# Optimization experiments

Measured on AMD Instinct MI355X. Metric: run time of the kernel, lower is better.

Reference implementation:

```python
import jax, jax.numpy as jnp
import numpy as np
import math

B, T, NC = 16, 256, 2
_NS = (9, 9, 11, 11, 9, 20)  # legacy6 region node counts
_OUT, _RF, _FD, _NH, _FF = 32, 64, 128, 4, 2048


def _region_adj(n):
    # chain + second-order edges (legacy6), plus self-loops; GCN sym-normalized
    A = np.zeros((n, n), np.float32)
    for i in range(n - 1):
        A[i, i + 1] = A[i + 1, i] = 1.0
    for i in range(n - 2):
        A[i, i + 2] = A[i + 2, i] = 1.0
    A = A + np.eye(n, dtype=np.float32)
    d = A.sum(1) ** -0.5
    return jnp.asarray(d[:, None] * A * d[None, :])

_ADJS = [_region_adj(n) for n in _NS]


def _pe_table(t, d):
    pos = np.arange(t, dtype=np.float32)[:, None]
    div = np.exp(np.arange(0, d, 2, dtype=np.float32) * (-math.log(10000.0) / d))
    pe = np.zeros((t, d), np.float32)
    pe[:, 0::2] = np.sin(pos * div)
    pe[:, 1::2] = np.cos(pos * div)
    return jnp.asarray(pe)

_PE = _pe_table(T, _FD)


def _ln(x, g, b, eps=1e-5):
    m = jnp.mean(x, -1, keepdims=True)
    v = jnp.mean((x - m) ** 2, -1, keepdims=True)
    return (x - m) / jnp.sqrt(v + eps) * g + b


def _mha(q, kv, qkv_w, qkv_b, ow, ob, nh):
    d = q.shape[-1]
    hd = d // nh
    wq, wk, wv = jnp.split(qkv_w, 3, axis=1)
    bq, bk, bv = jnp.split(qkv_b, 3)
    def sp(x):
        return x.reshape(x.shape[0], x.shape[1], nh, hd).transpose(0, 2, 1, 3)
    Q, K, V = sp(q @ wq + bq), sp(kv @ wk + bk), sp(kv @ wv + bv)
    att = jax.nn.softmax(jnp.einsum('bhqd,bhkd->bhqk', Q, K) / jnp.sqrt(jnp.float32(hd)), axis=-1)
    o = jnp.einsum('bhqk,bhkd->bhqd', att, V).transpose(0, 2, 1, 3).reshape(q.shape[0], q.shape[1], d)
    return o @ ow + ob


def _tel(x, qkv_w, qkv_b, ow, ob, l1g, l1b, f1w, f1b, f2w, f2b, l2g, l2b, nh):
    # torch post-norm TransformerEncoderLayer (relu FFN, eval mode: no dropout)
    x = _ln(x + _mha(x, x, qkv_w, qkv_b, ow, ob, nh), l1g, l1b)
    ff = jax.nn.relu(x @ f1w + f1b) @ f2w + f2b
    return _ln(x + ff, l2g, l2b)


def setup_inputs() -> dict:
    key = jax.random.key(0)
    ks = iter(jax.random.split(key, 80))
    def nrm(shape, s=0.05):
        return jax.random.normal(next(ks), shape, jnp.float32) * s
    inp = {}
    for name, n in zip(('x_ljaw', 'x_rjaw', 'x_leye', 'x_reye', 'x_nose', 'x_mouth'), _NS):
        inp[name] = jax.random.normal(next(ks), (B, T, n, 11), jnp.float32)
    inp['global_feats'] = jax.random.normal(next(ks), (B, T, 4), jnp.float32)
    inp['global_alpha'] = jnp.float32(0.2)
    inp['gcn1_w'] = nrm((6, 11, _OUT)); inp['gcn1_b'] = jnp.zeros((6, _OUT))
    inp['gcn2_w'] = nrm((6, _OUT, _OUT)); inp['gcn2_b'] = jnp.zeros((6, _OUT))
    inp['rln_g'] = jnp.ones((6, _RF)); inp['rln_b'] = jnp.zeros((6, _RF))
    inp['sp_qkv_w'] = nrm((_RF, 3 * _RF)); inp['sp_qkv_b'] = jnp.zeros((3 * _RF,))
    inp['sp_out_w'] = nrm((_RF, _RF)); inp['sp_out_b'] = jnp.zeros((_RF,))
    inp['sp_ln1_g'] = jnp.ones((_RF,)); inp['sp_ln1_b'] = jnp.zeros((_RF,))
    inp['sp_ff1_w'] = nrm((_RF, _FF)); inp['sp_ff1_b'] = jnp.zeros((_FF,))
    inp['sp_ff2_w'] = nrm((_FF, _RF)); inp['sp_ff2_b'] = jnp.zeros((_RF,))
    inp['sp_ln2_g'] = jnp.ones((_RF,)); inp['sp_ln2_b'] = jnp.zeros((_RF,))
    priors = np.array([0.3, 0.3, 0.8, 0.8, 0.4, 1.0], np.float32)
    inp['region_logits'] = jnp.asarray(np.log(np.expm1(priors)).reshape(1, 6, 1))
    inp['gate1_w'] = nrm((_RF, 32)); inp['gate1_b'] = jnp.zeros((32,))
    inp['gate2_w'] = nrm((32, 1)); inp['gate2_b'] = jnp.zeros((1,))
    inp['ca_qkv_w'] = nrm((_RF, 3 * _RF)); inp['ca_qkv_b'] = jnp.zeros((3 * _RF,))
    inp['ca_out_w'] = nrm((_RF, _RF)); inp['ca_out_b'] = jnp.zeros((_RF,))
    inp['ca_ln_g'] = jnp.ones((_RF,)); inp['ca_ln_b'] = jnp.zeros((_RF,))
    inp['glob_w'] = nrm((4, _RF)); inp['glob_b'] = jnp.zeros((_RF,))
    inp['glob_ln_g'] = jnp.ones((_RF,)); inp['glob_ln_b'] = jnp.zeros((_RF,))
    inp['fused_ln_g'] = jnp.ones((_FD,)); inp['fused_ln_b'] = jnp.zeros((_FD,))
    inp['tp_qkv_w'] = nrm((_FD, 3 * _FD)); inp['tp_qkv_b'] = jnp.zeros((3 * _FD,))
    inp['tp_out_w'] = nrm((_FD, _FD)); inp['tp_out_b'] = jnp.zeros((_FD,))
    inp['tp_ln1_g'] = jnp.ones((_FD,)); inp['tp_ln1_b'] = jnp.zeros((_FD,))
    inp['tp_ff1_w'] = nrm((_FD, _FF)); inp['tp_ff1_b'] = jnp.zeros((_FF,))
    inp['tp_ff2_w'] = nrm((_FF, _FD)); inp['tp_ff2_b'] = jnp.zeros((_FD,))
    inp['tp_ln2_g'] = jnp.ones((_FD,)); inp['tp_ln2_b'] = jnp.zeros((_FD,))
    inp['attnproj_w'] = nrm((_FD, 1)); inp['attnproj_b'] = jnp.zeros((1,))
    inp['cls1_w'] = nrm((_FD, _OUT)); inp['cls1_b'] = jnp.zeros((_OUT,))
    inp['cls_ln_g'] = jnp.ones((_OUT,)); inp['cls_ln_b'] = jnp.zeros((_OUT,))
    inp['cls2_w'] = nrm((_OUT, NC)); inp['cls2_b'] = jnp.zeros((NC,))
    return inp


def reference(x_ljaw, x_rjaw, x_leye, x_reye, x_nose, x_mouth, global_feats, global_alpha, gcn1_w, gcn1_b, gcn2_w, gcn2_b, rln_g, rln_b, sp_qkv_w, sp_qkv_b, sp_out_w, sp_out_b, sp_ln1_g, sp_ln1_b, sp_ff1_w, sp_ff1_b, sp_ff2_w, sp_ff2_b, sp_ln2_g, sp_ln2_b, region_logits, gate1_w, gate1_b, gate2_w, gate2_b, ca_qkv_w, ca_qkv_b, ca_out_w, ca_out_b, ca_ln_g, ca_ln_b, glob_w, glob_b, glob_ln_g, glob_ln_b, fused_ln_g, fused_ln_b, tp_qkv_w, tp_qkv_b, tp_out_w, tp_out_b, tp_ln1_g, tp_ln1_b, tp_ff1_w, tp_ff1_b, tp_ff2_w, tp_ff2_b, tp_ln2_g, tp_ln2_b, attnproj_w, attnproj_b, cls1_w, cls1_b, cls_ln_g, cls_ln_b, cls2_w, cls2_b):
    xs = (x_ljaw, x_rjaw, x_leye, x_reye, x_nose, x_mouth)
    Bc, Tc = x_ljaw.shape[0], x_ljaw.shape[1]
    # per-region 2-layer GCN + concat(mean,max) node pooling -> (B,T,64) tokens
    toks = []
    for i in range(6):
        A = _ADJS[i]
        h = jax.nn.relu(jnp.einsum('nm,btmf->btnf', A, xs[i] @ gcn1_w[i]) + gcn1_b[i])
        h = jax.nn.relu(jnp.einsum('nm,btmf->btnf', A, h @ gcn2_w[i]) + gcn2_b[i])
        feat = jnp.concatenate([h.mean(2), h.max(2)], -1)
        toks.append(_ln(feat, rln_g[i], rln_b[i]))
    tok = jnp.stack(toks, 2).reshape(Bc * Tc, 6, _RF)
    # spatial transformer over the 6 region tokens per frame
    tok = _tel(tok, sp_qkv_w, sp_qkv_b, sp_out_w, sp_out_b, sp_ln1_g, sp_ln1_b, sp_ff1_w, sp_ff1_b, sp_ff2_w, sp_ff2_b, sp_ln2_g, sp_ln2_b, _NH)
    # learned region priors (softplus) * per-sample sigmoid gates
    rw = jax.nn.softplus(region_logits)
    gate = jax.nn.sigmoid(jax.nn.relu(tok @ gate1_w + gate1_b) @ gate2_w + gate2_b)
    tok = tok * rw * gate
    # cross-attn fusion: mean-region query attends over region tokens
    q = jnp.mean(tok, 1, keepdims=True)
    attn = _mha(q, tok, ca_qkv_w, ca_qkv_b, ca_out_w, ca_out_b, _NH)
    fused_r = _ln(q[:, 0] + attn[:, 0], ca_ln_g, ca_ln_b)
    # gated global branch (4 -> 64), concat to fused_dim=128
    g = jax.nn.relu(_ln(global_feats.reshape(Bc * Tc, 4) @ glob_w + glob_b, glob_ln_g, glob_ln_b))
    g = jnp.tanh(global_alpha) * g
    fused = _ln(jnp.concatenate([fused_r, g], -1), fused_ln_g, fused_ln_b).reshape(Bc, Tc, _FD)
    # temporal transformer + attention pooling over time
    fused = fused + _PE[None, :Tc]
    h = _tel(fused, tp_qkv_w, tp_qkv_b, tp_out_w, tp_out_b, tp_ln1_g, tp_ln1_b, tp_ff1_w, tp_ff1_b, tp_ff2_w, tp_ff2_b, tp_ln2_g, tp_ln2_b, _NH)
    wt = jax.nn.softmax(h @ attnproj_w + attnproj_b, axis=1)
    pooled = jnp.sum(wt * h, 1)
    z = jax.nn.relu(_ln(pooled @ cls1_w + cls1_b, cls_ln_g, cls_ln_b))
    return z @ cls2_w + cls2_b
```

## Files before the change

### kernel.cpp

```cpp
#include <hip/hip_runtime.h>
#include <math.h>
#include <stddef.h>

#define NFRM 4096
#define NBATCH 16

typedef __attribute__((ext_vector_type(8))) short short8v;
typedef __attribute__((ext_vector_type(4))) float f32x4;
#define MFMA_BF16(a,b,c) __builtin_amdgcn_mfma_f32_16x16x32_bf16(a,b,c,0,0,0)

__device__ inline float wsum64(float v){
  #pragma unroll
  for(int m=32;m>=1;m>>=1) v += __shfl_xor(v, m, 64);
  return v;
}

__device__ inline float pe_val(int t,int d){
  int k = d >> 1;
  float div = expf(-(float)(2*k) * (9.210340371976184f/128.f));
  float ang = (float)t * div;
  return (d & 1) ? cosf(ang) : sinf(ang);
}

__device__ inline void bf16split(float x, unsigned short &h, unsigned short &l){
// ... 30 lines not shown
    const float* __restrict__ b1,
    const unsigned short* __restrict__ w2h, const unsigned short* __restrict__ w2l)
{
  constexpr int TM=32, JC=128;
  constexpr int KS1 = D/32;
  constexpr int NT2W = (D/16)/4;
  constexpr int HS = 2048/NS;
  constexpr int NCH = HS/JC;
  constexpr int HP = JC + 8;
  __shared__ unsigned short Hh[TM][HP];
  __shared__ unsigned short Hl[TM][HP];
  int tid = threadIdx.x;
  int lane = tid & 63, w = tid >> 6;
  int ar = lane & 15, ak = lane >> 4;
  size_t Ntok = (size_t)gridDim.x*TM;
  const float* Xb = X + (size_t)blockIdx.x*TM*D;

  short8v xah[2][KS1], xal[2][KS1];
  #pragma unroll
  for(int mt=0;mt<2;mt++){
    #pragma unroll
    for(int s=0;s<KS1;s++){
      const float* xp = Xb + (size_t)(mt*16+ar)*D + s*32 + ak*8;
      #pragma unroll
      for(int e=0;e<8;e++){
        unsigned short h,l;
        bf16split(xp[e],h,l);
        xah[mt][s][e]=(short)h; xal[mt][s][e]=(short)l;
      }
    }
  }

  f32x4 acc2[2][NT2W];
  #pragma unroll
  for(int mt=0;mt<2;mt++)
    #pragma unroll
    for(int nt=0;nt<NT2W;nt++)
      acc2[mt][nt] = (f32x4){0.f,0.f,0.f,0.f};

  for(int ch=0; ch<NCH; ch++){
    int jc = blockIdx.y*HS + ch*JC;
    f32x4 a1[2][2];
    #pragma unroll
    for(int mt=0;mt<2;mt++){ a1[mt][0]=(f32x4){0,0,0,0}; a1[mt][1]=(f32x4){0,0,0,0}; }
    #pragma unroll
    for(int s=0;s<KS1;s++){
      #pragma unroll
      for(int nt=0;nt<2;nt++){
        int ntile1 = (jc + w*32 + nt*16) >> 4;
        size_t off = (((size_t)ntile1*KS1 + s)*64 + lane)*8;
        short8v bh = *(const short8v*)(w1h + off);
        short8v bl = *(const short8v*)(w1l + off);
        #pragma unroll
        for(int mt=0;mt<2;mt++){
          a1[mt][nt] = MFMA_BF16(xah[mt][s], bh, a1[mt][nt]);
          a1[mt][nt] = MFMA_BF16(xah[mt][s], bl, a1[mt][nt]);
          a1[mt][nt] = MFMA_BF16(xal[mt][s], bh, a1[mt][nt]);
        }
      }
    }
    __syncthreads();
    #pragma unroll
    for(int nt=0;nt<2;nt++){
      int colBase = w*32 + nt*16 + ar;
      float bval = b1[jc + colBase];
      #pragma unroll
      for(int mt=0;mt<2;mt++){
        #pragma unroll
        for(int r=0;r<4;r++){
          float hv = a1[mt][nt][r] + bval;
          hv = fmaxf(hv, 0.f);
          unsigned short h,l;
          bf16split(hv,h,l);
          int row = mt*16 + ak*4 + r;
          Hh[row][colBase]=h; Hl[row][colBase]=l;
        }
      }
    }
    __syncthreads();
    #pragma unroll
    for(int s2=0;s2<4;s2++){
      short8v ah[2], al[2];
      #pragma unroll
      for(int mt=0;mt<2;mt++){
        ah[mt] = *(const short8v*)&Hh[mt*16+ar][s2*32 + ak*8];
        al[mt] = *(const short8v*)&Hl[mt*16+ar][s2*32 + ak*8];
      }
      #pragma unroll
      for(int nt=0;nt<NT2W;nt++){
        int ntile2 = w*NT2W + nt;
        int kstep2 = (jc >> 5) + s2;
        size_t off = (((size_t)ntile2*64 + kstep2)*64 + lane)*8;
        short8v bh = *(const short8v*)(w2h + off);
        short8v bl = *(const short8v*)(w2l + off);
        #pragma unroll
        for(int mt=0;mt<2;mt++){
          acc2[mt][nt] = MFMA_BF16(ah[mt], bh, acc2[mt][nt]);
          acc2[mt][nt] = MFMA_BF16(ah[mt], bl, acc2[mt][nt]);
          acc2[mt][nt] = MFMA_BF16(al[mt], bh, acc2[mt][nt]);
        }
      }
    }
  }
  float* Pb = P + (size_t)blockIdx.y*Ntok*D + (size_t)blockIdx.x*TM*D;
  #pragma unroll
  for(int mt=0;mt<2;mt++){
    #pragma unroll
    for(int nt=0;nt<NT2W;nt++){
      int col = (w*NT2W + nt)*16 + ar;
      #pragma unroll
      for(int r=0;r<4;r++){
        int row = mt*16 + ak*4 + r;
        Pb[(size_t)row*D + col] = acc2[mt][nt][r];
      }
    }
  }
}

template<int D, int NS>
__global__ __launch_bounds__(256) void ffn_combine_kernel(
    const float* __restrict__ X, const float* __restrict__ P,
    float* __restrict__ Y,
    const float* __restrict__ b2,
    const float* __restrict__ lg, const float* __restrict__ lb)
{
  constexpr int EPL = D/64;
  int tid=threadIdx.x;
  int lane = tid & 63;
  size_t Ntok = (size_t)gridDim.x*4;
  size_t row = (size_t)blockIdx.x*4 + (tid>>6);
  size_t base = row*D;
  float e[EPL];
  float s=0.f;
  #pragma unroll
  for(int i=0;i<EPL;i++){
    int c = i*64+lane;
    float v = X[base+c] + b2[c];
    #pragma unroll
    for(int sp=0;sp<NS;sp++) v += P[(size_t)sp*Ntok*D + base + c];
    e[i]=v; s+=v;
  }
  float mm = wsum64(s)*(1.f/D);
  float s2=0.f;
  #pragma unroll
  for(int i=0;i<EPL;i++){ float d=e[i]-mm; s2+=d*d; }
  float rs = rsqrtf(wsum64(s2)*(1.f/D)+1e-5f);
  #pragma unroll
  for(int i=0;i<EPL;i++){
    int c=i*64+lane;
    Y[base+c] = (e[i]-mm)*rs*lg[c]+lb[c];
  }
}

__global__ __launch_bounds__(64) void gcn_kernel(
    const float* __restrict__ x0,const float* __restrict__ x1,
    const float* __restrict__ x2,const float* __restrict__ x3,
    const float* __restrict__ x4,const float* __restrict__ x5,
    const float* __restrict__ g1w,const float* __restrict__ g1b,
    const float* __restrict__ g2w,const float* __restrict__ g2b,
    const float* __restrict__ rg,const float* __restrict__ rb,
    float* __restrict__ tok)
{
  int f = blockIdx.x;
  int r = blockIdx.y;
  int tid = threadIdx.x;
  int n = (r==5) ? 20 : ((r==2 || r==3) ? 11 : 9);
  const float* xr = (r==0)?x0:(r==1)?x1:(r==2)?x2:(r==3)?x3:(r==4)?x4:x5;
  const float* W1 = g1w + r*11*32;
  const float* b1 = g1b + r*32;
  const float* W2 = g2w + r*32*32;
  const float* b2 = g2b + r*32;

  __shared__ float xs[20*11];
  __shared__ float t0[20*32];
  __shared__ float t1[20*32];

  for(int i=tid;i<n*11;i+=64) xs[i] = xr[(size_t)f*n*11 + i];
  __syncthreads();
  for(int i=tid;i<n*32;i+=64){
    int node=i>>5, c=i&31;
    float s=0.f;
    #pragma unroll
    for(int k=0;k<11;k++) s += xs[node*11+k]*W1[k*32+c];
    t0[i]=s;
  }
  __syncthreads();
  for(int i=tid;i<n*32;i+=64){
    int node=i>>5, c=i&31;
    int di = 1 + min(node,2) + min(n-1-node,2);
    float s=b1[c];
    int lo = max(node-2,0), hi = min(node+2,n-1);
    for(int m=lo;m<=hi;m++){
      int dm = 1 + min(m,2) + min(n-1-m,2);
      s += rsqrtf((float)(di*dm)) * t0[m*32+c];
    }
    t1[i]=fmaxf(s,0.f);
  }
  __syncthreads();
  for(int i=tid;i<n*32;i+=64){
    int node=i>>5, c=i&31;
    float s=0.f;
    #pragma unroll
    for(int k=0;k<32;k++) s += t1[node*32+k]*W2[k*32+c];
    t0[i]=s;
  }
  __syncthreads();
  for(int i=tid;i<n*32;i+=64){
    int node=i>>5, c=i&31;
    int di = 1 + min(node,2) + min(n-1-node,2);
    float s=b2[c];
    int lo = max(node-2,0), hi = min(node+2,n-1);
    for(int m=lo;m<=hi;m++){
      int dm = 1 + min(m,2) + min(n-1-m,2);
      s += rsqrtf((float)(di*dm)) * t0[m*32+c];
    }
    t1[i]=fmaxf(s,0.f);
  }
  __syncthreads();
  float v;
  if(tid<32){
    float s=0.f;
    for(int m=0;m<n;m++) s += t1[m*32+tid];
    v = s/(float)n;
  } else {
    int c=tid-32;
    float mx=-1e30f;
    for(int m=0;m<n;m++) mx = fmaxf(mx, t1[m*32+c]);
    v = mx;
  }
  float m1 = wsum64(v)*(1.f/64.f);
  float d1 = v - m1;
  float var = wsum64(d1*d1)*(1.f/64.f);
  float y = d1*rsqrtf(var+1e-5f)*rg[r*64+tid] + rb[r*64+tid];
  tok[((size_t)f*6+r)*64+tid] = y;
}

__global__ __launch_bounds__(64) void sp_attn_kernel(
    float* __restrict__ tok,
    const float* __restrict__ qkvw,const float* __restrict__ qkvb,
    const float* __restrict__ ow,const float* __restrict__ ob,
    const float* __restrict__ l1g,const float* __restrict__ l1b)
{
  int f=blockIdx.x, tid=threadIdx.x;
  __shared__ float Xv[384];
  __shared__ float QKV[1152];
  __shared__ float SC[144];
  __shared__ float AO[384];
  __shared__ float Yv[384];
  float* trow = tok + (size_t)f*384;
  for(int i=tid;i<384;i+=64) Xv[i]=trow[i];
  __syncthreads();
  for(int i=tid;i<1152;i+=64){
    int tk=i/192, c=i%192;
    float s=qkvb[c];
    #pragma unroll
    for(int k=0;k<64;k++) s += Xv[tk*64+k]*qkvw[k*192+c];
    QKV[i]=s;
  }
  __syncthreads();
  for(int i=tid;i<144;i+=64){
    int h=i/36, qi=(i%36)/6, ki=i%6;
    float s=0.f;
    #pragma unroll
    for(int d=0;d<16;d++) s += QKV[qi*192+h*16+d]*QKV[ki*192+64+h*16+d];
    SC[i]=s*0.25f;
  }
  __syncthreads();
  if(tid<24){
    int base=(tid/6)*36+(tid%6)*6;
    float mx=-1e30f;
    for(int k=0;k<6;k++) mx=fmaxf(mx,SC[base+k]);
    float sm=0.f;
    for(int k=0;k<6;k++){ float e=expf(SC[base+k]-mx); SC[base+k]=e; sm+=e; }
    float rr=1.f/sm;
    for(int k=0;k<6;k++) SC[base+k]*=rr;
  }
  __syncthreads();
  for(int i=tid;i<384;i+=64){
    int tk=i/64, c=i%64, h=c/16;
    float s=0.f;
    #pragma unroll
    for(int k=0;k<6;k++) s += SC[h*36+tk*6+k]*QKV[k*192+128+c];
    AO[i]=s;
  }
  __syncthreads();
  for(int i=tid;i<384;i+=64){
    int tk=i/64, c=i%64;
    float s=ob[c];
    #pragma unroll
    for(int k=0;k<64;k++) s += AO[tk*64+k]*ow[k*64+c];
    Yv[i]=Xv[i]+s;
  }
  __syncthreads();
  #pragma unroll
  for(int row=0;row<6;row++){
    float v=Yv[row*64+tid];
    float mm=wsum64(v)*(1.f/64.f);
    float d=v-mm;
    float var=wsum64(d*d)*(1.f/64.f);
    trow[row*64+tid]=d*rsqrtf(var+1e-5f)*l1g[tid]+l1b[tid];
  }
}

template<int D, int TM>
__global__ __launch_bounds__(256) void ffn_ln_kernel(
    const float* __restrict__ X, float* __restrict__ Yout,
    const float* __restrict__ w1,const float* __restrict__ b1,
    const float* __restrict__ w2,const float* __restrict__ b2,
    const float* __restrict__ lg,const float* __restrict__ lb)
{
  constexpr int JC = 128;
  constexpr int JS = JC + 4;
  constexpr int M1 = TM/8;
  constexpr int CG = D/4;
  constexpr int MG2 = 256/CG;
  constexpr int M2 = TM/MG2;
  __shared__ float Xs[TM*D];
  __shared__ float Hs[TM*JS];
  int tid=threadIdx.x;
  const float* Xb = X + (size_t)blockIdx.x*TM*D;
  for(int i=tid;i<TM*D;i+=256) Xs[i]=Xb[i];

  int jg = tid & 31, j0 = jg*4;
  int mg1 = tid >> 5;
  int m10 = mg1*M1;
  int cg = tid % CG, c0 = cg*4;
  int mg2 = tid / CG;
  int m20 = mg2*M2;

  float acc[M2][4];
  #pragma unroll
  for(int m=0;m<M2;m++){ acc[m][0]=0.f;acc[m][1]=0.f;acc[m][2]=0.f;acc[m][3]=0.f; }

  __syncthreads();
  for(int jc=0;jc<2048;jc+=JC){
    float a1[M1][4];
    float4 bv = *(const float4*)&b1[jc+j0];
    #pragma unroll
    for(int m=0;m<M1;m++){ a1[m][0]=bv.x;a1[m][1]=bv.y;a1[m][2]=bv.z;a1[m][3]=bv.w; }
    for(int k0=0;k0<D;k0+=4){
      float4 wr0 = *(const float4*)&w1[(size_t)(k0+0)*2048 + jc + j0];
      float4 wr1 = *(const float4*)&w1[(size_t)(k0+1)*2048 + jc + j0];
      float4 wr2 = *(const float4*)&w1[(size_t)(k0+2)*2048 + jc + j0];
      float4 wr3 = *(const float4*)&w1[(size_t)(k0+3)*2048 + jc + j0];
      #pragma unroll
      for(int m=0;m<M1;m++){
        float4 xv = *(const float4*)&Xs[(m10+m)*D + k0];
        a1[m][0] += xv.x*wr0.x + xv.y*wr1.x + xv.z*wr2.x + xv.w*wr3.x;
        a1[m][1] += xv.x*wr0.y + xv.y*wr1.y + xv.z*wr2.y + xv.w*wr3.y;
        a1[m][2] += xv.x*wr0.z + xv.y*wr1.z + xv.z*wr2.z + xv.w*wr3.z;
        a1[m][3] += xv.x*wr0.w + xv.y*wr1.w + xv.z*wr2.w + xv.w*wr3.w;
      }
    }
    #pragma unroll
    for(int m=0;m<M1;m++){
      float4 hv;
      hv.x=fmaxf(a1[m][0],0.f); hv.y=fmaxf(a1[m][1],0.f);
      hv.z=fmaxf(a1[m][2],0.f); hv.w=fmaxf(a1[m][3],0.f);
      *(float4*)&Hs[(m10+m)*JS + j0] = hv;
    }
    __syncthreads();
    for(int jj0=0;jj0<JC;jj0+=4){
      float4 w20 = *(const float4*)&w2[(size_t)(jc+jj0+0)*D + c0];
      float4 w21 = *(const float4*)&w2[(size_t)(jc+jj0+1)*D + c0];
      float4 w22 = *(const float4*)&w2[(size_t)(jc+jj0+2)*D + c0];
      float4 w23 = *(const float4*)&w2[(size_t)(jc+jj0+3)*D + c0];
      #pragma unroll
      for(int m=0;m<M2;m++){
        float4 hv = *(const float4*)&Hs[(m20+m)*JS + jj0];
        acc[m][0] += hv.x*w20.x + hv.y*w21.x + hv.z*w22.x + hv.w*w23.x;
        acc[m][1] += hv.x*w20.y + hv.y*w21.y + hv.z*w22.y + hv.w*w23.y;
        acc[m][2] += hv.x*w20.z + hv.y*w21.z + hv.z*w22.z + hv.w*w23.z;
        acc[m][3] += hv.x*w20.w + hv.y*w21.w + hv.z*w22.w + hv.w*w23.w;
      }
    }
    __syncthreads();
  }
  {
    float4 b2v = *(const float4*)&b2[c0];
    #pragma unroll
    for(int m=0;m<M2;m++){
      int row = m20+m;
      float4 xv = *(const float4*)&Xs[row*D + c0];
      float4 yv;
      yv.x = xv.x + acc[m][0] + b2v.x;
      yv.y = xv.y + acc[m][1] + b2v.y;
      yv.z = xv.z + acc[m][2] + b2v.z;
      yv.w = xv.w + acc[m][3] + b2v.w;
      *(float4*)&Hs[row*D + c0] = yv;
    }
  }
  __syncthreads();
  constexpr int EPL = D/64;
  int lane = tid & 63, wv = tid >> 6;
  float* Yb = Yout + (size_t)blockIdx.x*TM*D;
  for(int row=wv; row<TM; row+=4){
    float e[EPL];
    float s=0.f;
    #pragma unroll
    for(int i=0;i<EPL;i++){ e[i]=Hs[row*D + i*64 + lane]; s+=e[i]; }
    float mm = wsum64(s)*(1.f/D);
    float s2=0.f;
    #pragma unroll
    for(int i=0;i<EPL;i++){ float d=e[i]-mm; s2+=d*d; }
    float rs = rsqrtf(wsum64(s2)*(1.f/D)+1e-5f);
    #pragma unroll
    for(int i=0;i<EPL;i++)
      Yb[row*D + i*64 + lane] = (e[i]-mm)*rs*lg[i*64+lane]+lb[i*64+lane];
  }
}

__global__ __launch_bounds__(64) void fuse_kernel(
    const float* __restrict__ tok, const float* __restrict__ gfeat,
    const float* __restrict__ alpha_p, const float* __restrict__ rlogit,
    const float* __restrict__ g1w,const float* __restrict__ g1b,
    const float* __restrict__ g2w,const float* __restrict__ g2b,
    const float* __restrict__ caqw,const float* __restrict__ caqb,
    const float* __restrict__ caow,const float* __restrict__ caob,
    const float* __restrict__ calng,const float* __restrict__ calnb,
    const float* __restrict__ gw,const float* __restrict__ gb,
    const float* __restrict__ glng,const float* __restrict__ glnb,
    const float* __restrict__ flng,const float* __restrict__ flnb,
    float* __restrict__ fused)
{
  int f=blockIdx.x, tid=threadIdx.x;
  __shared__ float X[384];
  __shared__ float G1[192];
  __shared__ float gt[6];
  __shared__ float qv[64];
  __shared__ float Qs[64];
  __shared__ float KK[384], VV[384];
  __shared__ float sc[24];
  __shared__ float AOs[64];

  const float* trow = tok + (size_t)f*384;
  for(int i=tid;i<384;i+=64) X[i]=trow[i];
  __syncthreads();
  for(int i=tid;i<192;i+=64){
    int rr=i/32, j=i%32;
    float s=g1b[j];
    #pragma unroll
    for(int k=0;k<64;k++) s += X[rr*64+k]*g1w[k*32+j];
    G1[i]=fmaxf(s,0.f);
  }
  __syncthreads();
  if(tid<6){
    float s=g2b[0];
    #pragma unroll
    for(int k=0;k<32;k++) s += G1[tid*32+k]*g2w[k];
    float gate = 1.f/(1.f+expf(-s));
    float rw = log1pf(expf(rlogit[tid]));
    gt[tid]=gate*rw;
  }
  __syncthreads();
  for(int i=tid;i<384;i+=64) X[i]*=gt[i/64];
  __syncthreads();
  {
    float s=0.f;
    #pragma unroll
    for(int rr=0;rr<6;rr++) s+=X[rr*64+tid];
    qv[tid]=s*(1.f/6.f);
  }
  __syncthreads();
  {
    float s=caqb[tid];
    #pragma unroll
    for(int k=0;k<64;k++) s += qv[k]*caqw[k*192+tid];
    Qs[tid]=s;
  }
  for(int i=tid;i<384;i+=64){
    int rr=i/64, c=i%64;
    float sk=caqb[64+c], sv=caqb[128+c];
    #pragma unroll
    for(int k=0;k<64;k++){
      float xv=X[rr*64+k];
      sk += xv*caqw[k*192+64+c];
      sv += xv*caqw[k*192+128+c];
    }
    KK[i]=sk; VV[i]=sv;
  }
  __syncthreads();
  if(tid<24){
    int h=tid/6, ki=tid%6;
    float s=0.f;
    #pragma unroll
    for(int d=0;d<16;d++) s += Qs[h*16+d]*KK[ki*64+h*16+d];
    sc[tid]=s*0.25f;
  }
  __syncthreads();
  if(tid<4){
    float mx=-1e30f;
    for(int k=0;k<6;k++) mx=fmaxf(mx,sc[tid*6+k]);
    float sm=0.f;
    for(int k=0;k<6;k++){ float e=expf(sc[tid*6+k]-mx); sc[tid*6+k]=e; sm+=e; }
    float rr=1.f/sm;
    for(int k=0;k<6;k++) sc[tid*6+k]*=rr;
  }
  __syncthreads();
  {
    int h=tid/16;
    float s=0.f;
    #pragma unroll
    for(int k=0;k<6;k++) s += sc[h*6+k]*VV[k*64+tid];
    AOs[tid]=s;
  }
  __syncthreads();
  float pr;
  {
    float s=caob[tid];
    #pragma unroll
    for(int k=0;k<64;k++) s += AOs[k]*caow[k*64+tid];
    pr = qv[tid] + s;
  }
  float m1=wsum64(pr)*(1.f/64.f);
  float d1=pr-m1;
  float v1=wsum64(d1*d1)*(1.f/64.f);
  float fr = d1*rsqrtf(v1+1e-5f)*calng[tid]+calnb[tid];
  float gvv;
  {
    float s=gb[tid];
    #pragma unroll
    for(int k=0;k<4;k++) s += gfeat[(size_t)f*4+k]*gw[k*64+tid];
    gvv=s;
  }
  float m2=wsum64(gvv)*(1.f/64.f);
  float d2=gvv-m2;
  float v2=wsum64(d2*d2)*(1.f/64.f);
  float gg = fmaxf(d2*rsqrtf(v2+1e-5f)*glng[tid]+glnb[tid],0.f)*tanhf(alpha_p[0]);
  float sm_ = wsum64(fr+gg)*(1.f/128.f);
  float da=fr-sm_, db=gg-sm_;
  float vv = wsum64(da*da+db*db)*(1.f/128.f);
  float rs = rsqrtf(vv+1e-5f);
  int t = f & 255;
  fused[(size_t)f*128+tid]     = da*rs*flng[tid]+flnb[tid]         + pe_val(t,tid);
  fused[(size_t)f*128+64+tid]  = db*rs*flng[64+tid]+flnb[64+tid]   + pe_val(t,64+tid);
}

__global__ __launch_bounds__(256) void tqkv_gemm_kernel(
    const float* __restrict__ X, float* __restrict__ Y,
    const float* __restrict__ w, const float* __restrict__ b)
{
  __shared__ float Xs[32*128];
  int tid=threadIdx.x;
  const float* Xb = X + (size_t)blockIdx.x*32*128;
  for(int i=tid;i<4096;i+=256) Xs[i]=Xb[i];
  __syncthreads();
  int cg = tid & 31, c0 = cg*4;
  int mg = tid >> 5, m0 = mg*4;
  float* Yb = Y + (size_t)blockIdx.x*32*384;
  int oc = blockIdx.y*128;
  float acc[4][4];
  float4 bv = *(const float4*)&b[oc+c0];
  #pragma unroll
  for(int m=0;m<4;m++){ acc[m][0]=bv.x;acc[m][1]=bv.y;acc[m][2]=bv.z;acc[m][3]=bv.w; }
  for(int k0=0;k0<128;k0+=4){
    float4 w0 = *(const float4*)&w[(k0+0)*384 + oc + c0];
    float4 w1 = *(const float4*)&w[(k0+1)*384 + oc + c0];
    float4 w2 = *(const float4*)&w[(k0+2)*384 + oc + c0];
    float4 w3 = *(const float4*)&w[(k0+3)*384 + oc + c0];
    #pragma unroll
    for(int m=0;m<4;m++){
      float4 xv = *(const float4*)&Xs[(m0+m)*128 + k0];
      acc[m][0] += xv.x*w0.x + xv.y*w1.x + xv.z*w2.x + xv.w*w3.x;
      acc[m][1] += xv.x*w0.y + xv.y*w1.y + xv.z*w2.y + xv.w*w3.y;
      acc[m][2] += xv.x*w0.z + xv.y*w1.z + xv.z*w2.z + xv.w*w3.z;
      acc[m][3] += xv.x*w0.w + xv.y*w1.w + xv.z*w2.w + xv.w*w3.w;
    }
  }
  #pragma unroll
  for(int m=0;m<4;m++){
    float4 yv; yv.x=acc[m][0];yv.y=acc[m][1];yv.z=acc[m][2];yv.w=acc[m][3];
    *(float4*)&Yb[(m0+m)*384 + oc + c0] = yv;
  }
}

__global__ __launch_bounds__(256) void tattn_split_kernel(
    const float* __restrict__ qkv, float* __restrict__ PO,
    float* __restrict__ PM, float* __restrict__ PL)
{
  int b=blockIdx.x, h=blockIdx.y, s=blockIdx.z, tid=threadIdx.x;
  __shared__ float Ksh[32*32];
  __shared__ float Vsh[32*32];
  const float* base = qkv + (size_t)b*256*384;
  int k0 = s*32;
  for(int i=tid;i<1024;i+=256){
    int t=i>>5, d=i&31;
    Ksh[i]=base[(size_t)(k0+t)*384+128+h*32+d];
    Vsh[i]=base[(size_t)(k0+t)*384+256+h*32+d];
  }
  float q[32];
  #pragma unroll
  for(int d=0;d<32;d++) q[d]=base[(size_t)tid*384+h*32+d];
  __syncthreads();
  const float scale=0.17677669529663687f;
  float sc[32];
  float mx=-1e30f;
  #pragma unroll
  for(int k=0;k<32;k++){
    float sv=0.f;
    #pragma unroll
    for(int d=0;d<32;d++) sv += q[d]*Ksh[k*32+d];
    sc[k]=sv*scale;
    mx=fmaxf(mx,sc[k]);
  }
  float l=0.f, o[32];
  #pragma unroll
  for(int d=0;d<32;d++) o[d]=0.f;
  #pragma unroll
  for(int k=0;k<32;k++){
    float p=expf(sc[k]-mx);
    l+=p;
    #pragma unroll
    for(int d=0;d<32;d++) o[d]+=p*Vsh[k*32+d];
  }
  int bh = b*4+h;
  size_t idx = ((size_t)s*64 + bh)*256 + tid;
  PM[idx]=mx; PL[idx]=l;
  float* po = PO + idx*32;
  #pragma unroll
  for(int d=0;d<32;d++) po[d]=o[d];
}

__global__ __launch_bounds__(256) void attn_combine_kernel(
    const float* __restrict__ PO, const float* __restrict__ PM,
    const float* __restrict__ PL, float* __restrict__ obuf)
{
  int tid=threadIdx.x;
  int ql = tid>>5, d = tid&31;
  int bh = blockIdx.x >> 5;
  int qc = blockIdx.x & 31;
  int q = qc*8 + ql;
  float ms[8], ls[8];
  float M=-1e30f;
  #pragma unroll
  for(int s=0;s<8;s++){
    size_t idx = ((size_t)s*64 + bh)*256 + q;
    ms[s]=PM[idx]; ls[s]=PL[idx];
    M=fmaxf(M,ms[s]);
  }
  float L=0.f, ov=0.f;
  #pragma unroll
  for(int s=0;s<8;s++){
    float w = expf(ms[s]-M);
    L += ls[s]*w;
    size_t idx = ((size_t)s*64 + bh)*256 + q;
    ov += w * PO[idx*32 + d];
  }
  int b = bh>>2, h = bh&3;
  obuf[(size_t)(b*256+q)*128 + h*32 + d] = ov / L;
}

__global__ __launch_bounds__(256) void tattn_kernel(
    const float* __restrict__ qkv, float* __restrict__ obuf)
{
  int b=blockIdx.x, h=blockIdx.y, tid=threadIdx.x;
  __shared__ float Ksh[256*32];
  __shared__ float Vsh[64*32];
  const float* base = qkv + (size_t)b*256*384;
  for(int i=tid;i<8192;i+=256){
    int t=i>>5, d=i&31;
    Ksh[i]=base[t*384+128+h*32+d];
  }
  float q[32];
  #pragma unroll
  for(int d=0;d<32;d++) q[d]=base[(size_t)tid*384+h*32+d];
  __syncthreads();
  const float scale=0.17677669529663687f;
  float mx=-1e30f;
  for(int k=0;k<256;k++){
    float s=0.f;
    #pragma unroll
    for(int d=0;d<32;d++) s += q[d]*Ksh[k*32+d];
    mx=fmaxf(mx,s*scale);
  }
  float l=0.f, o[32];
  #pragma unroll
  for(int d=0;d<32;d++) o[d]=0.f;
  for(int kc=0;kc<256;kc+=64){
    __syncthreads();
    for(int i=tid;i<2048;i+=256){
      int t=i>>5, d=i&31;
      Vsh[i]=base[(size_t)(kc+t)*384+256+h*32+d];
    }
    __syncthreads();
    for(int k2=0;k2<64;k2++){
      float s=0.f;
      #pragma unroll
      for(int d=0;d<32;d++) s += q[d]*Ksh[(kc+k2)*32+d];
// ... 75 lines not shown
  __shared__ float invs[1];
  __shared__ float pooled[128];
  __shared__ float z[32];
  const float* H = h2 + (size_t)b*256*128;
  {
    float s=apb[0];
    #pragma unroll
    for(int k=0;k<128;k++) s += H[(size_t)tid*128+k]*apw[k];
    lg[tid]=s;
  }
  __syncthreads();
  if(tid==0){
    float mx=-1e30f;
    for(int i=0;i<256;i++) mx=fmaxf(mx,lg[i]);
    float sm=0.f;
    for(int i=0;i<256;i++){ float e=expf(lg[i]-mx); wt[i]=e; sm+=e; }
    invs[0]=1.f/sm;
  }
  __syncthreads();
  float inv=invs[0];
  if(tid<128){
    float s=0.f;
    for(int t=0;t<256;t++) s += wt[t]*inv*H[(size_t)t*128+tid];
    pooled[tid]=s;
  }
  __syncthreads();
  if(tid<32){
    float s=c1b[tid];
    #pragma unroll
    for(int k=0;k<128;k++) s += pooled[k]*c1w[k*32+tid];
    z[tid]=s;
  }
  __syncthreads();
  if(tid==0){
    float m=0.f;
    for(int i=0;i<32;i++) m+=z[i];
    m *= (1.f/32.f);
    float v=0.f;
    for(int i=0;i<32;i++){ float d=z[i]-m; v+=d*d; }
    v *= (1.f/32.f);
    float rs=rsqrtf(v+1e-5f);
    for(int i=0;i<32;i++) z[i]=fmaxf((z[i]-m)*rs*clng[i]+clnb[i],0.f);
  }
  __syncthreads();
  if(tid<2){
    float s=c2b[tid];
    #pragma unroll
    for(int k=0;k<32;k++) s += z[k]*c2w[k*2+tid];
    out[b*2+tid]=s;
  }
}

extern "C" void kernel_launch(void* const* d_in, const int* in_sizes, int n_in,
                              void* d_out, int out_size, void* d_ws, size_t ws_size,
                              hipStream_t stream) {
  const float* x0 = (const float*)d_in[0];
  const float* x1 = (const float*)d_in[1];
  const float* x2 = (const float*)d_in[2];
  const float* x3 = (const float*)d_in[3];
  const float* x4 = (const float*)d_in[4];
  const float* x5 = (const float*)d_in[5];
  const float* gfeat   = (const float*)d_in[6];
  const float* alpha_p = (const float*)d_in[7];
  const float* g1w = (const float*)d_in[8];
  const float* g1b = (const float*)d_in[9];
  const float* g2w = (const float*)d_in[10];
  const float* g2b = (const float*)d_in[11];
  const float* rlg = (const float*)d_in[12];
  const float* rlb = (const float*)d_in[13];
  const float* spqkvw = (const float*)d_in[14];
  const float* spqkvb = (const float*)d_in[15];
  const float* spow = (const float*)d_in[16];
  const float* spob = (const float*)d_in[17];
  const float* spl1g = (const float*)d_in[18];
  const float* spl1b = (const float*)d_in[19];
  const float* spf1w = (const float*)d_in[20];
  const float* spf1b = (const float*)d_in[21];
  const float* spf2w = (const float*)d_in[22];
  const float* spf2b = (const float*)d_in[23];
  const float* spl2g = (const float*)d_in[24];
  const float* spl2b = (const float*)d_in[25];
  const float* rlogit = (const float*)d_in[26];
  const float* gate1w = (const float*)d_in[27];
  const float* gate1b = (const float*)d_in[28];
  const float* gate2w = (const float*)d_in[29];
  const float* gate2b = (const float*)d_in[30];
  const float* caqkvw = (const float*)d_in[31];
  const float* caqkvb = (const float*)d_in[32];
  const float* caow = (const float*)d_in[33];
  const float* caob = (const float*)d_in[34];
  const float* calng = (const float*)d_in[35];
  const float* calnb = (const float*)d_in[36];
  const float* globw = (const float*)d_in[37];
  const float* globb = (const float*)d_in[38];
  const float* glng = (const float*)d_in[39];
  const float* glnb = (const float*)d_in[40];
  const float* flng = (const float*)d_in[41];
  const float* flnb = (const float*)d_in[42];
  const float* tpqkvw = (const float*)d_in[43];
  const float* tpqkvb = (const float*)d_in[44];
  const float* tpow = (const float*)d_in[45];
  const float* tpob = (const float*)d_in[46];
  const float* tpl1g = (const float*)d_in[47];
  const float* tpl1b = (const float*)d_in[48];
  const float* tpf1w = (const float*)d_in[49];
  const float* tpf1b = (const float*)d_in[50];
  const float* tpf2w = (const float*)d_in[51];
  const float* tpf2b = (const float*)d_in[52];
  const float* tpl2g = (const float*)d_in[53];
  const float* tpl2b = (const float*)d_in[54];
  const float* apw = (const float*)d_in[55];
  const float* apb = (const float*)d_in[56];
  const float* c1w = (const float*)d_in[57];
  const float* c1b = (const float*)d_in[58];
  const float* clng = (const float*)d_in[59];
  const float* clnb = (const float*)d_in[60];
  const float* c2w = (const float*)d_in[61];
  const float* c2b = (const float*)d_in[62];

  float* ws = (float*)d_ws;
  float* tok   = ws;
  float* fused = tok   + (size_t)NFRM*384;
  float* qkv   = fused + (size_t)NFRM*128;
  float* obuf  = qkv   + (size_t)NFRM*384;
  float* part  = obuf  + (size_t)NFRM*128;
  size_t part_elems = (size_t)2*24576*64;
  unsigned short* pk = (unsigned short*)(part + part_elems);
  unsigned short* sp1h = pk;
  unsigned short* sp1l = sp1h + 131072;
  unsigned short* sp2h = sp1l + 131072;
  unsigned short* sp2l = sp2h + 131072;
  unsigned short* tp1h = sp2l + 131072;
  unsigned short* tp1l = tp1h + 262144;
  unsigned short* tp2h = tp1l + 262144;
  unsigned short* tp2l = tp2h + 262144;
  size_t pack_ushorts = 4*131072 + 4*262144;
  size_t need = ((size_t)NFRM*384 + NFRM*128 + NFRM*384 + NFRM*128 + part_elems)*4
              + pack_ushorts*2;
  bool mfma_ok = (ws_size >= need);

  float* attnPO = (float*)(pk + pack_ushorts);
  float* attnPM = attnPO + (size_t)8*64*256*32;
  float* attnPL = attnPM + (size_t)8*64*256;
  size_t need2 = need + ((size_t)8*64*256*32 + 2*(size_t)8*64*256)*4;
  bool attn_ok = (ws_size >= need2);

  if(mfma_ok){
    pack_w_kernel<<<dim3(128,2),64,0,stream>>>(spf1w, sp1h, sp1l, 64, 2048);
    pack_w_kernel<<<dim3(4,64),64,0,stream>>>(spf2w, sp2h, sp2l, 2048, 64);
    pack_w_kernel<<<dim3(128,4),64,0,stream>>>(tpf1w, tp1h, tp1l, 128, 2048);
    pack_w_kernel<<<dim3(8,64),64,0,stream>>>(tpf2w, tp2h, tp2l, 2048, 128);
  }

  gcn_kernel<<<dim3(NFRM,6),64,0,stream>>>(x0,x1,x2,x3,x4,x5,g1w,g1b,g2w,g2b,rlg,rlb,tok);
  sp_attn_kernel<<<NFRM,64,0,stream>>>(tok,spqkvw,spqkvb,spow,spob,spl1g,spl1b);
  if(mfma_ok){
    ffn_mfma_partial<64,2><<<dim3(768,2),256,0,stream>>>(tok,part,sp1h,sp1l,spf1b,sp2h,sp2l);
    ffn_combine_kernel<64,2><<<24576/4,256,0,stream>>>(tok,part,tok,spf2b,spl2g,spl2b);
  } else {
    ffn_ln_kernel<64,32><<<768,256,0,stream>>>(tok,tok,spf1w,spf1b,spf2w,spf2b,spl2g,spl2b);
  }
  fuse_kernel<<<NFRM,64,0,stream>>>(tok,gfeat,alpha_p,rlogit,gate1w,gate1b,gate2w,gate2b,
                                    caqkvw,caqkvb,caow,caob,calng,calnb,
                                    globw,globb,glng,glnb,flng,flnb,fused);
  tqkv_gemm_kernel<<<dim3(128,3),256,0,stream>>>(fused,qkv,tpqkvw,tpqkvb);
  if(attn_ok){
    tattn_split_kernel<<<dim3(NBATCH,4,8),256,0,stream>>>(qkv,attnPO,attnPM,attnPL);
    attn_combine_kernel<<<64*32,256,0,stream>>>(attnPO,attnPM,attnPL,obuf);
  } else {
    tattn_kernel<<<dim3(NBATCH,4),256,0,stream>>>(qkv,obuf);
  }
  tproj_gemm_kernel<<<128,256,0,stream>>>(obuf,fused,tpow,tpob,tpl1g,tpl1b);
  if(mfma_ok){
    ffn_mfma_partial<128,4><<<dim3(128,4),256,0,stream>>>(fused,part,tp1h,tp1l,tpf1b,tp2h,tp2l);
    ffn_combine_kernel<128,4><<<NFRM/4,256,0,stream>>>(fused,part,obuf,tpf2b,tpl2g,tpl2b);
  } else {
    ffn_ln_kernel<128,16><<<256,256,0,stream>>>(fused,obuf,tpf1w,tpf1b,tpf2w,tpf2b,tpl2g,tpl2b);
  }
  pool_cls_kernel<<<NBATCH,256,0,stream>>>(obuf,apw,apb,c1w,c1b,clng,clnb,c2w,c2b,(float*)d_out);
}
```

Measured before the change: 403.6 us.

## Batch four frames per block in GCN, spatial attention and fusion kernels

The GCN and fusion kernels now run four frames per 256-thread block, one wavefront per frame, with per-wave shared-memory slices. The spatial attention kernel processes four frames (24 tokens) together and computes the QKV and output projections as register-tiled GEMMs. Each weight load is then reused across several token rows, which cuts redundant global weight traffic and reduces the number of tiny 64-thread blocks. The cost is more shared memory per block, which can lower occupancy.

```diff
diff --git a/kernel.cpp b/kernel.cpp
--- a/kernel.cpp
+++ b/kernel.cpp
@@ -206,7 +206,7 @@
   }
 }
 
-__global__ __launch_bounds__(64) void gcn_kernel(
+__global__ __launch_bounds__(256) void gcn_kernel(
     const float* __restrict__ x0,const float* __restrict__ x1,
     const float* __restrict__ x2,const float* __restrict__ x3,
     const float* __restrict__ x4,const float* __restrict__ x5,
@@ -215,9 +215,10 @@
     const float* __restrict__ rg,const float* __restrict__ rb,
     float* __restrict__ tok)
 {
-  int f = blockIdx.x;
+  int tid=threadIdx.x;
+  int lane = tid & 63, w = tid >> 6;
+  int f = blockIdx.x*4 + w;
   int r = blockIdx.y;
-  int tid = threadIdx.x;
   int n = (r==5) ? 20 : ((r==2 || r==3) ? 11 : 9);
   const float* xr = (r==0)?x0:(r==1)?x1:(r==2)?x2:(r==3)?x3:(r==4)?x4:x5;
   const float* W1 = g1w + r*11*32;
@@ -225,134 +226,171 @@
   const float* W2 = g2w + r*32*32;
   const float* b2 = g2b + r*32;
 
-  __shared__ float xs[20*11];
-  __shared__ float t0[20*32];
-  __shared__ float t1[20*32];
-
-  for(int i=tid;i<n*11;i+=64) xs[i] = xr[(size_t)f*n*11 + i];
-  __syncthreads();
-  for(int i=tid;i<n*32;i+=64){
+  __shared__ float xs[4][220];
+  __shared__ float t0[4][640];
+  __shared__ float t1[4][640];
+
+  for(int i=lane;i<n*11;i+=64) xs[w][i] = xr[(size_t)f*n*11 + i];
+  __syncthreads();
+  for(int i=lane;i<n*32;i+=64){
     int node=i>>5, c=i&31;
     float s=0.f;
     #pragma unroll
-    for(int k=0;k<11;k++) s += xs[node*11+k]*W1[k*32+c];
-    t0[i]=s;
-  }
-  __syncthreads();
-  for(int i=tid;i<n*32;i+=64){
+    for(int k=0;k<11;k++) s += xs[w][node*11+k]*W1[k*32+c];
+    t0[w][i]=s;
+  }
+  __syncthreads();
+  for(int i=lane;i<n*32;i+=64){
     int node=i>>5, c=i&31;
     int di = 1 + min(node,2) + min(n-1-node,2);
     float s=b1[c];
     int lo = max(node-2,0), hi = min(node+2,n-1);
     for(int m=lo;m<=hi;m++){
       int dm = 1 + min(m,2) + min(n-1-m,2);
-      s += rsqrtf((float)(di*dm)) * t0[m*32+c];
-    }
-    t1[i]=fmaxf(s,0.f);
-  }
-  __syncthreads();
-  for(int i=tid;i<n*32;i+=64){
+      s += rsqrtf((float)(di*dm)) * t0[w][m*32+c];
+    }
+    t1[w][i]=fmaxf(s,0.f);
+  }
+  __syncthreads();
+  for(int i=lane;i<n*32;i+=64){
     int node=i>>5, c=i&31;
     float s=0.f;
     #pragma unroll
-    for(int k=0;k<32;k++) s += t1[node*32+k]*W2[k*32+c];
-    t0[i]=s;
-  }
-  __syncthreads();
-  for(int i=tid;i<n*32;i+=64){
+    for(int k=0;k<32;k++) s += t1[w][node*32+k]*W2[k*32+c];
+    t0[w][i]=s;
+  }
+  __syncthreads();
+  for(int i=lane;i<n*32;i+=64){
     int node=i>>5, c=i&31;
     int di = 1 + min(node,2) + min(n-1-node,2);
     float s=b2[c];
     int lo = max(node-2,0), hi = min(node+2,n-1);
     for(int m=lo;m<=hi;m++){
       int dm = 1 + min(m,2) + min(n-1-m,2);
-      s += rsqrtf((float)(di*dm)) * t0[m*32+c];
-    }
-    t1[i]=fmaxf(s,0.f);
+      s += rsqrtf((float)(di*dm)) * t0[w][m*32+c];
+    }
+    t1[w][i]=fmaxf(s,0.f);
   }
   __syncthreads();
   float v;
-  if(tid<32){
+  if(lane<32){
     float s=0.f;
-    for(int m=0;m<n;m++) s += t1[m*32+tid];
+    for(int m=0;m<n;m++) s += t1[w][m*32+lane];
     v = s/(float)n;
   } else {
-    int c=tid-32;
+    int c=lane-32;
     float mx=-1e30f;
-    for(int m=0;m<n;m++) mx = fmaxf(mx, t1[m*32+c]);
+    for(int m=0;m<n;m++) mx = fmaxf(mx, t1[w][m*32+c]);
     v = mx;
   }
   float m1 = wsum64(v)*(1.f/64.f);
   float d1 = v - m1;
   float var = wsum64(d1*d1)*(1.f/64.f);
-  float y = d1*rsqrtf(var+1e-5f)*rg[r*64+tid] + rb[r*64+tid];
-  tok[((size_t)f*6+r)*64+tid] = y;
-}
-
-__global__ __launch_bounds__(64) void sp_attn_kernel(
+  float y = d1*rsqrtf(var+1e-5f)*rg[r*64+lane] + rb[r*64+lane];
+  tok[((size_t)f*6+r)*64+lane] = y;
+}
+
+__global__ __launch_bounds__(256) void sp_attn_kernel(
     float* __restrict__ tok,
     const float* __restrict__ qkvw,const float* __restrict__ qkvb,
     const float* __restrict__ ow,const float* __restrict__ ob,
     const float* __restrict__ l1g,const float* __restrict__ l1b)
 {
-  int f=blockIdx.x, tid=threadIdx.x;
-  __shared__ float Xv[384];
-  __shared__ float QKV[1152];
-  __shared__ float SC[144];
-  __shared__ float AO[384];
-  __shared__ float Yv[384];
-  float* trow = tok + (size_t)f*384;
-  for(int i=tid;i<384;i+=64) Xv[i]=trow[i];
-  __syncthreads();
-  for(int i=tid;i<1152;i+=64){
-    int tk=i/192, c=i%192;
-    float s=qkvb[c];
-    #pragma unroll
-    for(int k=0;k<64;k++) s += Xv[tk*64+k]*qkvw[k*192+c];
-    QKV[i]=s;
-  }
-  __syncthreads();
-  for(int i=tid;i<144;i+=64){
-    int h=i/36, qi=(i%36)/6, ki=i%6;
+  __shared__ float Xs[24][64];
+  __shared__ float QKV[24][192];
+  __shared__ float SC[4][144];
+  __shared__ float AO[24][64];
+  int tid=threadIdx.x;
+  int f0 = blockIdx.x*4;
+  float* Xf = &Xs[0][0];
+  for(int i=tid;i<1536;i+=256) Xf[i] = tok[(size_t)f0*384 + i];
+  __syncthreads();
+  {
+    int cg = tid & 31, c0 = cg*6;
+    int rg = tid >> 5, r0 = rg*3;
+    float acc[3][6];
+    #pragma unroll
+    for(int m=0;m<3;m++)
+      #pragma unroll
+      for(int j=0;j<6;j++) acc[m][j]=qkvb[c0+j];
+    for(int k=0;k<64;k++){
+      float wv[6];
+      #pragma unroll
+      for(int j=0;j<6;j++) wv[j]=qkvw[k*192+c0+j];
+      float xv0=Xs[r0][k], xv1=Xs[r0+1][k], xv2=Xs[r0+2][k];
+      #pragma unroll
+      for(int j=0;j<6;j++){
+        acc[0][j]+=xv0*wv[j];
+        acc[1][j]+=xv1*wv[j];
+        acc[2][j]+=xv2*wv[j];
+      }
+    }
+    #pragma unroll
+    for(int m=0;m<3;m++)
+      #pragma unroll
+      for(int j=0;j<6;j++) QKV[r0+m][c0+j]=acc[m][j];
+  }
+  __syncthreads();
+  for(int i=tid;i<576;i+=256){
+    int fr=i/144, rest=i%144;
+    int h=rest/36, qi=(rest%36)/6, ki=rest%6;
     float s=0.f;
     #pragma unroll
-    for(int d=0;d<16;d++) s += QKV[qi*192+h*16+d]*QKV[ki*192+64+h*16+d];
-    SC[i]=s*0.25f;
-  }
-  __syncthreads();
-  if(tid<24){
-    int base=(tid/6)*36+(tid%6)*6;
+    for(int d=0;d<16;d++) s += QKV[fr*6+qi][h*16+d]*QKV[fr*6+ki][64+h*16+d];
+    SC[fr][rest]=s*0.25f;
+  }
+  __syncthreads();
+  if(tid<96){
+    int fr=tid/24, idx=tid%24;
+    int base=idx*6;
     float mx=-1e30f;
-    for(int k=0;k<6;k++) mx=fmaxf(mx,SC[base+k]);
+    for(int k=0;k<6;k++) mx=fmaxf(mx,SC[fr][base+k]);
     float sm=0.f;
-    for(int k=0;k<6;k++){ float e=expf(SC[base+k]-mx); SC[base+k]=e; sm+=e; }
+    for(int k=0;k<6;k++){ float e=expf(SC[fr][base+k]-mx); SC[fr][base+k]=e; sm+=e; }
     float rr=1.f/sm;
-    for(int k=0;k<6;k++) SC[base+k]*=rr;
-  }
-  __syncthreads();
-  for(int i=tid;i<384;i+=64){
-    int tk=i/64, c=i%64, h=c/16;
+    for(int k=0;k<6;k++) SC[fr][base+k]*=rr;
+  }
+  __syncthreads();
+  for(int i=tid;i<1536;i+=256){
+    int fr=i/384, rem=i%384;
+    int row=rem/64, c=rem&63, h=c/16;
     float s=0.f;
     #pragma unroll
-    for(int k=0;k<6;k++) s += SC[h*36+tk*6+k]*QKV[k*192+128+c];
-    AO[i]=s;
-  }
-  __syncthreads();
-  for(int i=tid;i<384;i+=64){
-    int tk=i/64, c=i%64;
-    float s=ob[c];
-    #pragma unroll
-    for(int k=0;k<64;k++) s += AO[tk*64+k]*ow[k*64+c];
-    Yv[i]=Xv[i]+s;
-  }
-  __syncthreads();
-  #pragma unroll
-  for(int row=0;row<6;row++){
-    float v=Yv[row*64+tid];
-    float mm=wsum64(v)*(1.f/64.f);
-    float d=v-mm;
-    float var=wsum64(d*d)*(1.f/64.f);
-    trow[row*64+tid]=d*rsqrtf(var+1e-5f)*l1g[tid]+l1b[tid];
+    for(int k=0;k<6;k++) s += SC[fr][h*36+row*6+k]*QKV[fr*6+k][128+c];
+    AO[fr*6+row][c]=s;
+  }
+  __syncthreads();
+  {
+    int cg = tid & 31, c0 = cg*2;
+    int rg = tid >> 5, r0 = rg*3;
+    float acc[3][2];
+    #pragma unroll
+    for(int m=0;m<3;m++){ acc[m][0]=ob[c0]; acc[m][1]=ob[c0+1]; }
+    for(int k=0;k<64;k++){
+      float w0=ow[k*64+c0], w1=ow[k*64+c0+1];
+      float a0=AO[r0][k], a1=AO[r0+1][k], a2=AO[r0+2][k];
+      acc[0][0]+=a0*w0; acc[0][1]+=a0*w1;
+      acc[1][0]+=a1*w0; acc[1][1]+=a1*w1;
+      acc[2][0]+=a2*w0; acc[2][1]+=a2*w1;
+    }
+    #pragma unroll
+    for(int m=0;m<3;m++){
+      QKV[r0+m][c0]   = Xs[r0+m][c0]   + acc[m][0];
+      QKV[r0+m][c0+1] = Xs[r0+m][c0+1] + acc[m][1];
+    }
+  }
+  __syncthreads();
+  {
+    int lane = tid & 63, w = tid >> 6;
+    #pragma unroll
+    for(int rr=0;rr<6;rr++){
+      int row = w*6+rr;
+      float v=QKV[row][lane];
+      float mm=wsum64(v)*(1.f/64.f);
+      float d=v-mm;
+      float var=wsum64(d*d)*(1.f/64.f);
+      tok[(size_t)f0*384 + row*64 + lane]=d*rsqrtf(var+1e-5f)*l1g[lane]+l1b[lane];
+    }
   }
 }
 
@@ -464,7 +502,7 @@
   }
 }
 
-__global__ __launch_bounds__(64) void fuse_kernel(
+__global__ __launch_bounds__(256) void fuse_kernel(
     const float* __restrict__ tok, const float* __restrict__ gfeat,
     const float* __restrict__ alpha_p, const float* __restrict__ rlogit,
     const float* __restrict__ g1w,const float* __restrict__ g1b,
@@ -477,117 +515,119 @@
     const float* __restrict__ flng,const float* __restrict__ flnb,
     float* __restrict__ fused)
 {
-  int f=blockIdx.x, tid=threadIdx.x;
-  __shared__ float X[384];
-  __shared__ float G1[192];
-  __shared__ float gt[6];
-  __shared__ float qv[64];
-  __shared__ float Qs[64];
-  __shared__ float KK[384], VV[384];
-  __shared__ float sc[24];
-  __shared__ float AOs[64];
+  int tid=threadIdx.x;
+  int lane = tid & 63, w = tid >> 6;
+  int f = blockIdx.x*4 + w;
+  __shared__ float X[4][384];
+  __shared__ float G1[4][192];
+  __shared__ float gt[4][6];
+  __shared__ float qv[4][64];
+  __shared__ float Qs[4][64];
+  __shared__ float KK[4][384], VV[4][384];
+  __shared__ float sc[4][24];
+  __shared__ float AOs[4][64];
 
   const float* trow = tok + (size_t)f*384;
-  for(int i=tid;i<384;i+=64) X[i]=trow[i];
-  __syncthreads();
-  for(int i=tid;i<192;i+=64){
+  for(int i=lane;i<384;i+=64) X[w][i]=trow[i];
+  __syncthreads();
+  for(int i=lane;i<192;i+=64){
     int rr=i/32, j=i%32;
     float s=g1b[j];
     #pragma unroll
-    for(int k=0;k<64;k++) s += X[rr*64+k]*g1w[k*32+j];
-    G1[i]=fmaxf(s,0.f);
-  }
-  __syncthreads();
-  if(tid<6){
+    for(int k=0;k<64;k++) s += X[w][rr*64+k]*g1w[k*32+j];
+    G1[w][i]=fmaxf(s,0.f);
+  }
+  __syncthreads();
+  if(lane<6){
     float s=g2b[0];
     #pragma unroll
-    for(int k=0;k<32;k++) s += G1[tid*32+k]*g2w[k];
+    for(int k=0;k<32;k++) s += G1[w][lane*32+k]*g2w[k];
     float gate = 1.f/(1.f+expf(-s));
-    float rw = log1pf(expf(rlogit[tid]));
-    gt[tid]=gate*rw;
-  }
-  __syncthreads();
-  for(int i=tid;i<384;i+=64) X[i]*=gt[i/64];
+    float rw = log1pf(expf(rlogit[lane]));
+    gt[w][lane]=gate*rw;
+  }
+  __syncthreads();
+  for(int i=lane;i<384;i+=64) X[w][i]*=gt[w][i/64];
   __syncthreads();
   {
     float s=0.f;
     #pragma unroll
-    for(int rr=0;rr<6;rr++) s+=X[rr*64+tid];
-    qv[tid]=s*(1.f/6.f);
+    for(int rr=0;rr<6;rr++) s+=X[w][rr*64+lane];
+    qv[w][lane]=s*(1.f/6.f);
   }
   __syncthreads();
   {
-    float s=caqb[tid];
-    #pragma unroll
-    for(int k=0;k<64;k++) s += qv[k]*caqw[k*192+tid];
-    Qs[tid]=s;
-  }
-  for(int i=tid;i<384;i+=64){
+    float s=caqb[lane];
+    #pragma unroll
+    for(int k=0;k<64;k++) s += qv[w][k]*caqw[k*192+lane];
+    Qs[w][lane]=s;
+  }
+  for(int i=lane;i<384;i+=64){
     int rr=i/64, c=i%64;
     float sk=caqb[64+c], sv=caqb[128+c];
     #pragma unroll
     for(int k=0;k<64;k++){
-      float xv=X[rr*64+k];
+      float xv=X[w][rr*64+k];
       sk += xv*caqw[k*192+64+c];
       sv += xv*caqw[k*192+128+c];
     }
-    KK[i]=sk; VV[i]=sv;
-  }
-  __syncthreads();
-  if(tid<24){
-    int h=tid/6, ki=tid%6;
+    KK[w][i]=sk; VV[w][i]=sv;
+  }
+  __syncthreads();
+  if(lane<24){
+    int h=lane/6, ki=lane%6;
     float s=0.f;
     #pragma unroll
-    for(int d=0;d<16;d++) s += Qs[h*16+d]*KK[ki*64+h*16+d];
-    sc[tid]=s*0.25f;
-  }
-  __syncthreads();
-  if(tid<4){
+    for(int d=0;d<16;d++) s += Qs[w][h*16+d]*KK[w][ki*64+h*16+d];
+    sc[w][lane]=s*0.25f;
+  }
+  __syncthreads();
+  if(lane<4){
     float mx=-1e30f;
-    for(int k=0;k<6;k++) mx=fmaxf(mx,sc[tid*6+k]);
+    for(int k=0;k<6;k++) mx=fmaxf(mx,sc[w][lane*6+k]);
     float sm=0.f;
-    for(int k=0;k<6;k++){ float e=expf(sc[tid*6+k]-mx); sc[tid*6+k]=e; sm+=e; }
+    for(int k=0;k<6;k++){ float e=expf(sc[w][lane*6+k]-mx); sc[w][lane*6+k]=e; sm+=e; }
     float rr=1.f/sm;
-    for(int k=0;k<6;k++) sc[tid*6+k]*=rr;
+    for(int k=0;k<6;k++) sc[w][lane*6+k]*=rr;
   }
   __syncthreads();
   {
-    int h=tid/16;
+    int h=lane/16;
     float s=0.f;
     #pragma unroll
-    for(int k=0;k<6;k++) s += sc[h*6+k]*VV[k*64+tid];
-    AOs[tid]=s;
+    for(int k=0;k<6;k++) s += sc[w][h*6+k]*VV[w][k*64+lane];
+    AOs[w][lane]=s;
   }
   __syncthreads();
   float pr;
   {
-    float s=caob[tid];
-    #pragma unroll
-    for(int k=0;k<64;k++) s += AOs[k]*caow[k*64+tid];
-    pr = qv[tid] + s;
+    float s=caob[lane];
+    #pragma unroll
+    for(int k=0;k<64;k++) s += AOs[w][k]*caow[k*64+lane];
+    pr = qv[w][lane] + s;
   }
   float m1=wsum64(pr)*(1.f/64.f);
   float d1=pr-m1;
   float v1=wsum64(d1*d1)*(1.f/64.f);
-  float fr = d1*rsqrtf(v1+1e-5f)*calng[tid]+calnb[tid];
+  float fr = d1*rsqrtf(v1+1e-5f)*calng[lane]+calnb[lane];
   float gvv;
   {
-    float s=gb[tid];
-    #pragma unroll
-    for(int k=0;k<4;k++) s += gfeat[(size_t)f*4+k]*gw[k*64+tid];
+    float s=gb[lane];
+    #pragma unroll
+    for(int k=0;k<4;k++) s += gfeat[(size_t)f*4+k]*gw[k*64+lane];
     gvv=s;
   }
   float m2=wsum64(gvv)*(1.f/64.f);
   float d2=gvv-m2;
   float v2=wsum64(d2*d2)*(1.f/64.f);
-  float gg = fmaxf(d2*rsqrtf(v2+1e-5f)*glng[tid]+glnb[tid],0.f)*tanhf(alpha_p[0]);
+  float gg = fmaxf(d2*rsqrtf(v2+1e-5f)*glng[lane]+glnb[lane],0.f)*tanhf(alpha_p[0]);
   float sm_ = wsum64(fr+gg)*(1.f/128.f);
   float da=fr-sm_, db=gg-sm_;
   float vv = wsum64(da*da+db*db)*(1.f/128.f);
   float rs = rsqrtf(vv+1e-5f);
   int t = f & 255;
-  fused[(size_t)f*128+tid]     = da*rs*flng[tid]+flnb[tid]         + pe_val(t,tid);
-  fused[(size_t)f*128+64+tid]  = db*rs*flng[64+tid]+flnb[64+tid]   + pe_val(t,64+tid);
+  fused[(size_t)f*128+lane]     = da*rs*flng[lane]+flnb[lane]         + pe_val(t,lane);
+  fused[(size_t)f*128+64+lane]  = db*rs*flng[64+lane]+flnb[64+lane]   + pe_val(t,64+lane);
 }
 
 __global__ __launch_bounds__(256) void tqkv_gemm_kernel(
@@ -969,15 +1009,15 @@
     pack_w_kernel<<<dim3(8,64),64,0,stream>>>(tpf2w, tp2h, tp2l, 2048, 128);
   }
 
-  gcn_kernel<<<dim3(NFRM,6),64,0,stream>>>(x0,x1,x2,x3,x4,x5,g1w,g1b,g2w,g2b,rlg,rlb,tok);
-  sp_attn_kernel<<<NFRM,64,0,stream>>>(tok,spqkvw,spqkvb,spow,spob,spl1g,spl1b);
+  gcn_kernel<<<dim3(NFRM/4,6),256,0,stream>>>(x0,x1,x2,x3,x4,x5,g1w,g1b,g2w,g2b,rlg,rlb,tok);
+  sp_attn_kernel<<<NFRM/4,256,0,stream>>>(tok,spqkvw,spqkvb,spow,spob,spl1g,spl1b);
   if(mfma_ok){
     ffn_mfma_partial<64,2><<<dim3(768,2),256,0,stream>>>(tok,part,sp1h,sp1l,spf1b,sp2h,sp2l);
     ffn_combine_kernel<64,2><<<24576/4,256,0,stream>>>(tok,part,tok,spf2b,spl2g,spl2b);
   } else {
     ffn_ln_kernel<64,32><<<768,256,0,stream>>>(tok,tok,spf1w,spf1b,spf2w,spf2b,spl2g,spl2b);
   }
-  fuse_kernel<<<NFRM,64,0,stream>>>(tok,gfeat,alpha_p,rlogit,gate1w,gate1b,gate2w,gate2b,
+  fuse_kernel<<<NFRM/4,256,0,stream>>>(tok,gfeat,alpha_p,rlogit,gate1w,gate1b,gate2w,gate2b,
                                     caqkvw,caqkvb,caow,caob,calng,calnb,
                                     globw,globb,glng,glnb,flng,flnb,fused);
   tqkv_gemm_kernel<<<dim3(128,3),256,0,stream>>>(fused,qkv,tpqkvw,tpqkvb);
```

Measured after the change: 358.1 us. -11.3%, faster.
